# Kernel tuning notes

Hardware: AMD Instinct MI355X
Metric: run time of the kernel (lower is better)

Reference implementation:

```python
import jax, jax.numpy as jnp
import numpy as np

N = 64000      # total nodes in batched graph (16 graphs x 4000)
E = 1024000    # total edges (avg degree 16)
D = 512        # input/output feature dim
KTOT = 2048    # total assign dim (128 clusters per graph)
B = 16         # batch size (number of graphs)


def setup_inputs() -> dict:
    key = jax.random.key(0)
    ks = jax.random.split(key, 5)
    feat = jax.random.normal(ks[0], (N, D), jnp.float32)
    W_feat = jax.random.normal(ks[1], (D, D), jnp.float32) / np.float32(np.sqrt(D))
    b_feat = jnp.zeros((D,), jnp.float32)
    W_pool = jax.random.normal(ks[2], (D, KTOT), jnp.float32) / np.float32(np.sqrt(D))
    b_pool = jnp.zeros((KTOT,), jnp.float32)
    src = jax.random.randint(ks[3], (E,), 0, N, dtype=jnp.int32)
    dst = jax.random.randint(ks[4], (E,), 0, N, dtype=jnp.int32)
    return {"feat": feat, "W_feat": W_feat, "b_feat": b_feat,
            "W_pool": W_pool, "b_pool": b_pool,
            "src": src, "dst": dst, "batch_size": B}


def _gin(x, src, dst, W, b):
    """GIN layer with mean aggregator: relu(W @ (x + mean_neighbors(x)) + b)."""
    n = x.shape[0]
    agg = jax.ops.segment_sum(x[src], dst, num_segments=n)              # [N, d_in]
    deg = jax.ops.segment_sum(jnp.ones((src.shape[0],), x.dtype), dst, num_segments=n)
    agg = agg / jnp.maximum(deg, 1.0)[:, None]
    return jax.nn.relu((x + agg) @ W + b)


def reference(feat, W_feat, b_feat, W_pool, b_pool, src, dst, batch_size):
    n = feat.shape[0]
    ktot = W_pool.shape[1]
    n_per = n // batch_size      # equal-sized graphs (batch_num_nodes)
    k_per = ktot // batch_size   # clusters per graph

    h_feat = _gin(feat, src, dst, W_feat, b_feat)    # [N, D]
    assign = _gin(feat, src, dst, W_pool, b_pool)    # [N, KTOT]

    # block_diag mask: node of graph b may only assign to columns of graph b
    gid_node = jnp.arange(n) // n_per                # [N]
    gid_col = jnp.arange(ktot) // k_per              # [KTOT]
    mask = (gid_node[:, None] == gid_col[None, :]).astype(assign.dtype)

    # allennlp masked_softmax(memory_efficient=False):
    # softmax(x * mask) * mask, renormalized with +1e-13
    s = jax.nn.softmax(assign * mask, axis=-1) * mask
    s = s / (s.sum(axis=-1, keepdims=True) + 1e-13)  # [N, KTOT]

    h = s.T @ h_feat                                 # [KTOT, D]
    # sparse adj @ S via edge-list scatter: (A S)[i] = sum_{(i,j) in E} S[j]
    adj_s = jax.ops.segment_sum(s[dst], src, num_segments=n)  # [N, KTOT]
    adj_new = s.T @ adj_s                            # [KTOT, KTOT]
    return adj_new, h
```

## Files before the change

### kernel.cpp

```cpp
#include <hip/hip_runtime.h>
#include <math.h>

constexpr int N  = 64000;
constexpr int E  = 1024000;
constexpr int D  = 512;
constexpr int KT = 2048;
constexpr int B  = 16;
constexpr int NP = 4000;
constexpr int KP = 128;
constexpr int NR = N / 256;
constexpr int EPB = 2048;
constexpr int NPB = E / EPB;
constexpr int RSTRIDE = 4608;
constexpr int BSTRIDE = 4608;

typedef __attribute__((ext_vector_type(4))) float f32x4;
typedef __attribute__((ext_vector_type(2))) float f32x2;
typedef __attribute__((ext_vector_type(8))) short bf16x8;
typedef __attribute__((ext_vector_type(8))) unsigned short u16x8;

__device__ __forceinline__ unsigned short f2bf(float f) {
    unsigned u = __builtin_bit_cast(unsigned, f);
    return (unsigned short)((u + 0x7FFFu + ((u >> 16) & 1u)) >> 16);
}
__device__ __forceinline__ float bf2f(unsigned short h) {
    unsigned u = (unsigned)h << 16;
    return __builtin_bit_cast(float, u);
}

__device__ __forceinline__ unsigned char f2fp8_sw(float f) {
    unsigned u = __builtin_bit_cast(unsigned, f);
    unsigned s = u >> 31;
    float a = fabsf(f);
    if (a > 448.f) a = 448.f;
    unsigned code;
    if (a < 0.015625f) {
        code = (unsigned)rintf(a * 512.0f);
    } else {
        unsigned au = __builtin_bit_cast(unsigned, a);
        unsigned mant = au & 0x7FFFFFu;
        unsigned rnd = 0x7FFFFu + ((mant >> 20) & 1u);
        unsigned r2 = au + rnd;
        int e = (int)(r2 >> 23) - 127;
        unsigned m3 = (r2 >> 20) & 7u;
        if (e > 8) { e = 8; m3 = 7; }
        code = (unsigned)((e + 7) << 3) | m3;
    }
    return (unsigned char)(code | (s << 7));
}
__device__ __forceinline__ float fp82f_sw(unsigned b) {
    unsigned s = b >> 7, e = (b >> 3) & 15u, m = b & 7u;
    float vn = __builtin_bit_cast(float, ((e + 120u) << 23) | (m << 20));
    float vs = (float)(int)m * 0x1p-9f;
    float v = e ? vn : vs;
    return s ? -v : v;
}

__device__ __forceinline__ unsigned pack4_fp8(float f0, float f1, float f2, float f3) {
#if __has_builtin(__builtin_amdgcn_cvt_pk_fp8_f32)
    int w = __builtin_amdgcn_cvt_pk_fp8_f32(f0, f1, 0, false);
    w = __builtin_amdgcn_cvt_pk_fp8_f32(f2, f3, w, true);
    return (unsigned)w;
#else
    return (unsigned)f2fp8_sw(f0) | ((unsigned)f2fp8_sw(f1) << 8) |
           ((unsigned)f2fp8_sw(f2) << 16) | ((unsigned)f2fp8_sw(f3) << 24);
#endif
}

__device__ __forceinline__ void acc8_fp8(float* a, uint2 w) {
#if __has_builtin(__builtin_amdgcn_cvt_pk_f32_fp8)
    f32x2 p0 = __builtin_amdgcn_cvt_pk_f32_fp8((int)w.x, false);
    f32x2 p1 = __builtin_amdgcn_cvt_pk_f32_fp8((int)w.x, true);
    f32x2 p2 = __builtin_amdgcn_cvt_pk_f32_fp8((int)w.y, false);
    f32x2 p3 = __builtin_amdgcn_cvt_pk_f32_fp8((int)w.y, true);
    a[0] += p0.x; a[1] += p0.y; a[2] += p1.x; a[3] += p1.y;
    a[4] += p2.x; a[5] += p2.y; a[6] += p3.x; a[7] += p3.y;
#else
    #pragma unroll
    for (int q = 0; q < 4; ++q) a[q] += fp82f_sw((w.x >> (8 * q)) & 255u);
    #pragma unroll
    for (int q = 0; q < 4; ++q) a[4 + q] += fp82f_sw((w.y >> (8 * q)) & 255u);
#endif
}

typedef const __attribute__((address_space(1))) unsigned int* gas_u32p;
typedef __attribute__((address_space(3))) unsigned int* las_u32p;
__device__ __forceinline__ void glds16(const unsigned short* g, unsigned short* l) {
    __builtin_amdgcn_global_load_lds((gas_u32p)(const void*)g, (las_u32p)(void*)l, 16, 0, 0);
}

__device__ __forceinline__ int block_incl_scan(int v, int* ws) {
    int t = threadIdx.x, lane = t & 63, w = t >> 6;
    int x = v;
    #pragma unroll
    for (int off = 1; off < 64; off <<= 1) {
        int y = __shfl_up(x, off);
        if (lane >= off) x += y;
    }
    if (lane == 63) ws[w] = x;
    __syncthreads();
    if (t < 4) {
        int s = ws[t];
        #pragma unroll
        for (int off = 1; off < 4; off <<= 1) {
            int y = __shfl_up(s, off);
            if (t >= off) s += y;
        }
        ws[t] = s;
    }
    __syncthreads();
    return x + (w > 0 ? ws[w - 1] : 0);
}

__global__ __launch_bounds__(256) void k_cvt(const float* __restrict__ in,
                                             unsigned short* __restrict__ outb,
                                             unsigned char* __restrict__ out8,
                                             long long n) {
    long long i = ((long long)blockIdx.x * 256 + threadIdx.x) * 8;
    if (i >= n) return;
    f32x4 a = *(const f32x4*)&in[i];
    f32x4 b = *(const f32x4*)&in[i + 4];
    u16x8 o;
    o[0] = f2bf(a.x); o[1] = f2bf(a.y); o[2] = f2bf(a.z); o[3] = f2bf(a.w);
    o[4] = f2bf(b.x); o[5] = f2bf(b.y); o[6] = f2bf(b.z); o[7] = f2bf(b.w);
    *(u16x8*)&outb[i] = o;
    uint2 w;
    w.x = pack4_fp8(a.x, a.y, a.z, a.w);
    w.y = pack4_fp8(b.x, b.y, b.z, b.w);
    *(uint2*)&out8[i] = w;
}

__global__ void k_zrow(unsigned short* __restrict__ fb,
                       unsigned short* __restrict__ scb,
                       unsigned short* __restrict__ hfb,
                       unsigned char* __restrict__ f8b) {
    int t = threadIdx.x;
    const u16x8 Z = {0, 0, 0, 0, 0, 0, 0, 0};
    if (t < 64)        *(u16x8*)&fb[(size_t)N * D + t * 8] = Z;
    else if (t < 80)   *(u16x8*)&scb[(size_t)N * KP + (t - 64) * 8] = Z;
    else if (t < 144)  *(u16x8*)&hfb[(size_t)N * D + (t - 80) * 8] = Z;
    else if (t < 176)  *(u16x8*)&f8b[(size_t)N * D + (size_t)(t - 144) * 16] = Z;
}

__global__ __launch_bounds__(256) void k_transpose(const float* __restrict__ in,
                                                   unsigned short* __restrict__ out,
                                                   int R, int C) {
    __shared__ float tile[32][33];
    int bx = blockIdx.x * 32, by = blockIdx.y * 32;
    int tx = threadIdx.x & 31, ty = threadIdx.x >> 5;
    #pragma unroll
    for (int i = 0; i < 32; i += 8)
        if (by + ty + i < R && bx + tx < C)
            tile[ty + i][tx] = in[(size_t)(by + ty + i) * C + bx + tx];
    __syncthreads();
    #pragma unroll
    for (int i = 0; i < 32; i += 8)
        if (bx + ty + i < C && by + tx < R)
            out[(size_t)(bx + ty + i) * R + by + tx] = f2bf(tile[tx][ty + i]);
}

__global__ void k_init(int* __restrict__ rcur, int* __restrict__ bcur) {
    int t = threadIdx.x;
    if (t < NR) rcur[t] = t * RSTRIDE;
    bcur[t] = t * BSTRIDE;
}

__global__ __launch_bounds__(256) void k_split(const int* __restrict__ src,
                                               const int* __restrict__ dst,
                                               int* __restrict__ rcur, int2* __restrict__ out1,
                                               int* __restrict__ bcur, int2* __restrict__ out2) {
    __shared__ int2 stg[EPB];
    __shared__ int h[256], lstart[256], gbase[256];
    __shared__ int ws[4];
    int t = threadIdx.x;
    int e0 = blockIdx.x * EPB;
    int sv[8], dv[8], bin[8], rank[8];
    #pragma unroll
    for (int i = 0; i < 8; ++i) {
        int e = e0 + t + i * 256;
        sv[i] = src[e]; dv[i] = dst[e];
    }
    h[t] = 0;
    __syncthreads();
    #pragma unroll
    for (int i = 0; i < 8; ++i) {
        bin[i] = dv[i] >> 8;
        rank[i] = atomicAdd(&h[bin[i]], 1);
    }
    __syncthreads();
    {
        int v = h[t];
        int incl = block_incl_scan(v, ws);
        lstart[t] = incl - v;
        gbase[t] = v ? atomicAdd(&rcur[t], v) : 0;
    }
    __syncthreads();
    #pragma unroll
    for (int i = 0; i < 8; ++i)
        stg[lstart[bin[i]] + rank[i]] = int2{sv[i], dv[i]};
    __syncthreads();
    for (int i = t; i < EPB; i += 256) {
        int2 e = stg[i];
        int b = e.y >> 8;
        out1[gbase[b] + i - lstart[b]] = e;
    }
    __syncthreads();
    h[t] = 0;
    __syncthreads();
    #pragma unroll
    for (int i = 0; i < 8; ++i) {
        bin[i] = (sv[i] / NP) * B + dv[i] / NP;
        rank[i] = atomicAdd(&h[bin[i]], 1);
    }
    __syncthreads();
    {
        int v = h[t];
        int incl = block_incl_scan(v, ws);
        lstart[t] = incl - v;
        gbase[t] = v ? atomicAdd(&bcur[t], v) : 0;
    }
    __syncthreads();
    #pragma unroll
    for (int i = 0; i < 8; ++i)
        stg[lstart[bin[i]] + rank[i]] = int2{sv[i], dv[i]};
    __syncthreads();
    for (int i = t; i < EPB; i += 256) {
        int2 e = stg[i];
        int b = (e.x / NP) * B + e.y / NP;
        out2[gbase[b] + i - lstart[b]] = e;
    }
}

__global__ __launch_bounds__(256) void k_part2(const int2* __restrict__ pairs,
                                               const int* __restrict__ rcur,
                                               int* __restrict__ rowstart,
                                               int* __restrict__ degv,
                                               int* __restrict__ csr) {
    __shared__ int h[256];
    __shared__ int ws[4];
    int t = threadIdx.x;
    int r = blockIdx.x;
    int p0 = r * RSTRIDE, p1 = rcur[r];
    h[t] = 0;
    __syncthreads();
    for (int p = p0 + t; p < p1; p += 256)
        atomicAdd(&h[pairs[p].y & 255], 1);
    __syncthreads();
    int v = h[t];
    int incl = block_incl_scan(v, ws);
    int start = p0 + incl - v;
    __syncthreads();
    h[t] = start;
    rowstart[r * 256 + t] = start;
    degv[r * 256 + t] = v;
    __syncthreads();
    for (int p = p0 + t; p < p1; p += 256) {
        int2 e = pairs[p];
        int pos = atomicAdd(&h[e.y & 255], 1);
        csr[pos] = e.x;
    }
}

__global__ __launch_bounds__(256) void k_agg(const unsigned short* __restrict__ fb,
                                             const unsigned char* __restrict__ f8,
                                             const int* __restrict__ rowstart,
                                             const int* __restrict__ degv,
                                             const int* __restrict__ csr,
                                             unsigned short* __restrict__ xb) {
    int w = threadIdx.x >> 6, lane = threadIdx.x & 63;
    int node = blockIdx.x * 4 + w;
    int r0 = rowstart[node], dg = degv[node], r1 = r0 + dg;
    u16x8 self = *(const u16x8*)&fb[(size_t)node * D + lane * 8];
    float a[8] = {};
    for (int base = r0; base < r1; base += 64) {
        int ii = base + lane;
        int idx = N;
        if (ii < r1) idx = csr[ii];
        int cnt = r1 - base; if (cnt > 64) cnt = 64;
        int batches = (cnt + 7) & ~7;
        for (int j = 0; j < batches; j += 8) {
            int s0 = __shfl(idx, j + 0), s1 = __shfl(idx, j + 1);
            int s2 = __shfl(idx, j + 2), s3 = __shfl(idx, j + 3);
            int s4 = __shfl(idx, j + 4), s5 = __shfl(idx, j + 5);
            int s6 = __shfl(idx, j + 6), s7 = __shfl(idx, j + 7);
            uint2 g0 = *(const uint2*)&f8[(size_t)s0 * D + lane * 8];
            uint2 g1 = *(const uint2*)&f8[(size_t)s1 * D + lane * 8];
            uint2 g2 = *(const uint2*)&f8[(size_t)s2 * D + lane * 8];
            uint2 g3 = *(const uint2*)&f8[(size_t)s3 * D + lane * 8];
            uint2 g4 = *(const uint2*)&f8[(size_t)s4 * D + lane * 8];
            uint2 g5 = *(const uint2*)&f8[(size_t)s5 * D + lane * 8];
            uint2 g6 = *(const uint2*)&f8[(size_t)s6 * D + lane * 8];
            uint2 g7 = *(const uint2*)&f8[(size_t)s7 * D + lane * 8];
            acc8_fp8(a, g0); acc8_fp8(a, g1); acc8_fp8(a, g2); acc8_fp8(a, g3);
            acc8_fp8(a, g4); acc8_fp8(a, g5); acc8_fp8(a, g6); acc8_fp8(a, g7);
        }
    }
    float inv = 1.0f / fmaxf((float)dg, 1.0f);
    u16x8 o;
    #pragma unroll
    for (int q = 0; q < 8; ++q) o[q] = f2bf(bf2f(self[q]) + a[q] * inv);
    *(u16x8*)&xb[(size_t)node * D + lane * 8] = o;
}

__global__ __launch_bounds__(256) void k_gemm_feat(const unsigned short* __restrict__ Xb,
                                                   const unsigned short* __restrict__ Wt,
                                                   const float* __restrict__ bias,
                                                   unsigned short* __restrict__ Hf) {
    __shared__ unsigned short As[128 * 64];
    __shared__ unsigned short Bs[128 * 64];
    int t = threadIdx.x, wid = t >> 6, lane = t & 63;
    int wm = wid >> 1, wn = wid & 1;
    int row0 = blockIdx.x * 128, col0 = blockIdx.y * 128;
    int r8 = lane >> 3, ch = (lane & 7) ^ r8;
    f32x4 acc[4][4] = {};
    for (int k0 = 0; k0 < D; k0 += 64) {
        #pragma unroll
        for (int i = 0; i < 4; ++i) {
            int rr = wid * 32 + i * 8;
            glds16(Xb + (size_t)(row0 + rr + r8) * D + k0 + ch * 8, As + rr * 64);
            glds16(Wt + (size_t)(col0 + rr + r8) * D + k0 + ch * 8, Bs + rr * 64);
        }
        __syncthreads();
        #pragma unroll
        for (int ks = 0; ks < 2; ++ks) {
            bf16x8 af[4], bfr[4];
            #pragma unroll
            for (int f = 0; f < 4; ++f) {
                int ra = wm * 64 + f * 16 + (lane & 15);
                af[f] = *(const bf16x8*)&As[ra * 64 + (((ks * 4 + (lane >> 4)) ^ (ra & 7)) << 3)];
                int rb = wn * 64 + f * 16 + (lane & 15);
                bfr[f] = *(const bf16x8*)&Bs[rb * 64 + (((ks * 4 + (lane >> 4)) ^ (rb & 7)) << 3)];
            }
            #pragma unroll
            for (int m = 0; m < 4; ++m)
                #pragma unroll
                for (int n = 0; n < 4; ++n)
                    acc[m][n] = __builtin_amdgcn_mfma_f32_16x16x32_bf16(af[m], bfr[n], acc[m][n], 0, 0, 0);
        }
        __syncthreads();
    }
    float bv[4];
    #pragma unroll
    for (int n = 0; n < 4; ++n) bv[n] = bias[col0 + wn * 64 + n * 16 + (lane & 15)];
    #pragma unroll
    for (int m = 0; m < 4; ++m)
        #pragma unroll
        for (int r = 0; r < 4; ++r) {
            int row = row0 + wm * 64 + m * 16 + (lane >> 4) * 4 + r;
            #pragma unroll
            for (int n = 0; n < 4; ++n) {
                int col = col0 + wn * 64 + n * 16 + (lane & 15);
                float v = fmaxf(acc[m][n][r] + bv[n], 0.f);
                Hf[(size_t)row * D + col] = f2bf(v);
            }
        }
}

__global__ __launch_bounds__(256) void k_gemm_pool(const unsigned short* __restrict__ Xb,
                                                   const unsigned short* __restrict__ Wpt,
                                                   const float* __restrict__ bp,
                                                   unsigned short* __restrict__ sc) {
    __shared__ unsigned short As[128 * 64];
    __shared__ unsigned short Bs[128 * 64];
    int t = threadIdx.x, wid = t >> 6, lane = t & 63;
    int bm = blockIdx.x;
    int g  = blockIdx.y;
    int row0 = g * NP + bm * 128;
    int nrows = NP - bm * 128; if (nrows > 128) nrows = 128;
    int col0 = g * KP;
    int r8 = lane >> 3, ch = (lane & 7) ^ r8;
    f32x4 acc[2][8] = {};
    for (int k0 = 0; k0 < D; k0 += 64) {
        #pragma unroll
        for (int i = 0; i < 4; ++i) {
            int rr = wid * 32 + i * 8;
            glds16(Xb + (size_t)(row0 + rr + r8) * D + k0 + ch * 8, As + rr * 64);
            glds16(Wpt + (size_t)(col0 + rr + r8) * D + k0 + ch * 8, Bs + rr * 64);
        }
        __syncthreads();
        #pragma unroll
        for (int ks = 0; ks < 2; ++ks) {
            bf16x8 af[2], bfr[8];
            #pragma unroll
            for (int m = 0; m < 2; ++m) {
                int ra = wid * 32 + m * 16 + (lane & 15);
                af[m] = *(const bf16x8*)&As[ra * 64 + (((ks * 4 + (lane >> 4)) ^ (ra & 7)) << 3)];
            }
            #pragma unroll
            for (int n = 0; n < 8; ++n) {
                int rb = n * 16 + (lane & 15);
                bfr[n] = *(const bf16x8*)&Bs[rb * 64 + (((ks * 4 + (lane >> 4)) ^ (rb & 7)) << 3)];
            }
            #pragma unroll
            for (int m = 0; m < 2; ++m)
                #pragma unroll
                for (int n = 0; n < 8; ++n)
                    acc[m][n] = __builtin_amdgcn_mfma_f32_16x16x32_bf16(af[m], bfr[n], acc[m][n], 0, 0, 0);
        }
        __syncthreads();
    }
    float bv[8];
    #pragma unroll
    for (int n = 0; n < 8; ++n) bv[n] = bp[col0 + n * 16 + (lane & 15)];
    #pragma unroll
    for (int m = 0; m < 2; ++m)
        #pragma unroll
        for (int r = 0; r < 4; ++r) {
            float v[8];
            #pragma unroll
            for (int n = 0; n < 8; ++n) v[n] = fmaxf(acc[m][n][r] + bv[n], 0.f);
            float mx = v[0];
            #pragma unroll
            for (int n = 1; n < 8; ++n) mx = fmaxf(mx, v[n]);
            #pragma unroll
            for (int off = 1; off < 16; off <<= 1) mx = fmaxf(mx, __shfl_xor(mx, off));
            float ssum = 0.f;
            #pragma unroll
            for (int n = 0; n < 8; ++n) { v[n] = __expf(v[n] - mx); ssum += v[n]; }
            #pragma unroll
            for (int off = 1; off < 16; off <<= 1) ssum += __shfl_xor(ssum, off);
            float inv = 1.0f / ssum;
            int rowl = wid * 32 + m * 16 + (lane >> 4) * 4 + r;
            if (rowl < nrows) {
                #pragma unroll
                for (int n = 0; n < 8; ++n)
                    sc[(size_t)(row0 + rowl) * KP + n * 16 + (lane & 15)] = f2bf(v[n] * inv);
            }
        }
}

constexpr int VBASE = 4128;

__device__ __forceinline__ void uv_write(unsigned short* arr, int c0, int es,
                                         const u16x8& l0, const u16x8& l1,
                                         const u16x8& l2, const u16x8& l3) {
    #pragma unroll
    for (int q = 0; q < 8; ++q) {
        int r0 = c0 + q, r1 = c0 + 8 + q, r2 = c0 + 16 + q, r3 = c0 + 24 + q;
        arr[r0 * 32 + (es ^ (((r0 >> 1) & 3) << 3))] = l0[q];
        arr[r1 * 32 + (es ^ (((r1 >> 1) & 3) << 3))] = l1[q];
        arr[r2 * 32 + (es ^ (((r2 >> 1) & 3) << 3))] = l2[q];
        arr[r3 * 32 + (es ^ (((r3 >> 1) & 3) << 3))] = l3[q];
    }
}

__device__ __forceinline__ void row_load(const unsigned short* row,
                                         u16x8& l0, u16x8& l1, u16x8& l2, u16x8& l3) {
    l0 = *(const u16x8*)(row);
    l1 = *(const u16x8*)(row + 8);
    l2 = *(const u16x8*)(row + 16);
    l3 = *(const u16x8*)(row + 24);
}

__device__ __forceinline__ bf16x8 uv_read(const unsigned short* UV, int base,
                                          int row, int chunk) {
    int c = chunk ^ ((row >> 1) & 3);
    return *(const bf16x8*)&UV[base + row * 32 + c * 8];
}

constexpr int KZ_H = 16;
__global__ __launch_bounds__(256) void k_h(const unsigned short* __restrict__ sc,
                                           const unsigned short* __restrict__ hf,
                                           float* __restrict__ outH) {
    __shared__ __align__(16) unsigned short UV[8224];
    int t = threadIdx.x, wid = t >> 6, lane = t & 63;
    int g  = blockIdx.x;
    int nt = blockIdx.y;
    int kz = blockIdx.z;
    int n0 = nt * 128;
    int i0 = g * NP + kz * (NP / KZ_H), i1 = i0 + NP / KZ_H;
    int c0 = wid * 32;
    int es = lane & 31, op = lane >> 5;
    unsigned short* arr = &UV[op * VBASE];
    f32x4 acc[2][8] = {};

    const unsigned short* baseptr = op ? (hf + n0 + c0) : (sc + c0);
    int rstride = op ? D : KP;
    auto mkrow = [&](int tbase) -> const unsigned short* {
        int nd = tbase + es;
        nd = nd < i1 ? nd : N;
        return baseptr + (size_t)nd * rstride;
    };

    u16x8 a0, a1, a2, a3, b0, b1, b2, b3;
    row_load(mkrow(i0), a0, a1, a2, a3);
    row_load(mkrow(i0 + 32), b0, b1, b2, b3);

    int ntile = (i1 - i0 + 31) >> 5;
    for (int tt = 0; tt < ntile; tt += 2) {
        __syncthreads();
        uv_write(arr, c0, es, a0, a1, a2, a3);
        __syncthreads();
        row_load(mkrow(i0 + (tt + 2) * 32), a0, a1, a2, a3);
        {
            bf16x8 af[2], bfr[8];
            #pragma unroll
            for (int m = 0; m < 2; ++m)
                af[m] = uv_read(UV, 0, wid * 32 + m * 16 + (lane & 15), lane >> 4);
            #pragma unroll
            for (int n = 0; n < 8; ++n)
                bfr[n] = uv_read(UV, VBASE, n * 16 + (lane & 15), lane >> 4);
            #pragma unroll
            for (int m = 0; m < 2; ++m)
                #pragma unroll
                for (int n = 0; n < 8; ++n)
                    acc[m][n] = __builtin_amdgcn_mfma_f32_16x16x32_bf16(af[m], bfr[n], acc[m][n], 0, 0, 0);
        }
        __syncthreads();
        uv_write(arr, c0, es, b0, b1, b2, b3);
        __syncthreads();
        row_load(mkrow(i0 + (tt + 3) * 32), b0, b1, b2, b3);
        {
            bf16x8 af[2], bfr[8];
            #pragma unroll
            for (int m = 0; m < 2; ++m)
                af[m] = uv_read(UV, 0, wid * 32 + m * 16 + (lane & 15), lane >> 4);
            #pragma unroll
            for (int n = 0; n < 8; ++n)
                bfr[n] = uv_read(UV, VBASE, n * 16 + (lane & 15), lane >> 4);
            #pragma unroll
            for (int m = 0; m < 2; ++m)
                #pragma unroll
                for (int n = 0; n < 8; ++n)
                    acc[m][n] = __builtin_amdgcn_mfma_f32_16x16x32_bf16(af[m], bfr[n], acc[m][n], 0, 0, 0);
        }
    }
    #pragma unroll
    for (int m = 0; m < 2; ++m)
        #pragma unroll
        for (int r = 0; r < 4; ++r) {
            int row = g * KP + wid * 32 + m * 16 + (lane >> 4) * 4 + r;
            #pragma unroll
            for (int n = 0; n < 8; ++n) {
                int col = n0 + n * 16 + (lane & 15);
                atomicAdd(&outH[(size_t)row * D + col], acc[m][n][r]);
            }
        }
}

constexpr int ADJ_SPLIT = 4;
__global__ __launch_bounds__(256) void k_adj(const unsigned short* __restrict__ sc,
                                             const int2* __restrict__ bpairs,
                                             const int* __restrict__ bcur,
                                             float* __restrict__ outA) {
    __shared__ __align__(16) unsigned short UV[8224];
    int t = threadIdx.x, wid = t >> 6, lane = t & 63;
    int b = blockIdx.x, part = blockIdx.y;
    int g1 = b >> 4, g2 = b & 15;
    int e0 = b * BSTRIDE, e1 = bcur[b], cnt = e1 - e0;
    int s0 = e0 + (int)((long long)cnt * part / ADJ_SPLIT);
    int s1 = e0 + (int)((long long)cnt * (part + 1) / ADJ_SPLIT);
    int c0 = wid * 32;
    int es = lane & 31, op = lane >> 5;
    unsigned short* arr = &UV[op * VBASE];
    f32x4 acc[2][8] = {};

    auto mkrow = [&](int tbase) -> const unsigned short* {
        int idx = tbase + es;
        bool v = idx < s1;
        int2 e = bpairs[v ? idx : s0];
        int node = v ? (op ? e.y : e.x) : N;
        return sc + (size_t)node * KP + c0;
    };

    u16x8 a0, a1, a2, a3, b0, b1, b2, b3;
    row_load(mkrow(s0), a0, a1, a2, a3);
    row_load(mkrow(s0 + 32), b0, b1, b2, b3);

    int ntile = (s1 - s0 + 31) >> 5;
    for (int tt = 0; tt < ntile; tt += 2) {
        __syncthreads();
        uv_write(arr, c0, es, a0, a1, a2, a3);
        __syncthreads();
        row_load(mkrow(s0 + (tt + 2) * 32), a0, a1, a2, a3);
        {
            bf16x8 af[2], bfr[8];
            #pragma unroll
            for (int m = 0; m < 2; ++m)
                af[m] = uv_read(UV, 0, wid * 32 + m * 16 + (lane & 15), lane >> 4);
            #pragma unroll
            for (int n = 0; n < 8; ++n)
                bfr[n] = uv_read(UV, VBASE, n * 16 + (lane & 15), lane >> 4);
            #pragma unroll
            for (int m = 0; m < 2; ++m)
                #pragma unroll
                for (int n = 0; n < 8; ++n)
                    acc[m][n] = __builtin_amdgcn_mfma_f32_16x16x32_bf16(af[m], bfr[n], acc[m][n], 0, 0, 0);
        }
        __syncthreads();
        uv_write(arr, c0, es, b0, b1, b2, b3);
        __syncthreads();
        row_load(mkrow(s0 + (tt + 3) * 32), b0, b1, b2, b3);
        {
            bf16x8 af[2], bfr[8];
            #pragma unroll
            for (int m = 0; m < 2; ++m)
                af[m] = uv_read(UV, 0, wid * 32 + m * 16 + (lane & 15), lane >> 4);
            #pragma unroll
            for (int n = 0; n < 8; ++n)
                bfr[n] = uv_read(UV, VBASE, n * 16 + (lane & 15), lane >> 4);
            #pragma unroll
            for (int m = 0; m < 2; ++m)
                #pragma unroll
                for (int n = 0; n < 8; ++n)
                    acc[m][n] = __builtin_amdgcn_mfma_f32_16x16x32_bf16(af[m], bfr[n], acc[m][n], 0, 0, 0);
        }
    }
    #pragma unroll
    for (int m = 0; m < 2; ++m)
        #pragma unroll
        for (int r = 0; r < 4; ++r) {
            int row = g1 * KP + wid * 32 + m * 16 + (lane >> 4) * 4 + r;
            #pragma unroll
            for (int n = 0; n < 8; ++n) {
                int col = g2 * KP + n * 16 + (lane & 15);
                atomicAdd(&outA[(size_t)row * KT + col], acc[m][n][r]);
            }
        }
}

extern "C" void kernel_launch(void* const* d_in, const int* in_sizes, int n_in,
                              void* d_out, int out_size, void* d_ws, size_t ws_size,
                              hipStream_t stream) {
    const float* feat   = (const float*)d_in[0];
    const float* W_feat = (const float*)d_in[1];
    const float* b_feat = (const float*)d_in[2];
    const float* W_pool = (const float*)d_in[3];
    const float* b_pool = (const float*)d_in[4];
    const int*   src    = (const int*)d_in[5];
    const int*   dst    = (const int*)d_in[6];

    char* w = (char*)d_ws;
    unsigned short* fb  = (unsigned short*)w; w += (size_t)(N + 1) * D * 2;
    unsigned char*  f8b = (unsigned char*)w;  w += (size_t)(N + 1) * D;
    unsigned short* xb  = (unsigned short*)w; w += (size_t)N * D * 2;
    unsigned short* hfb = (unsigned short*)w; w += (size_t)(N + 1) * D * 2;
    unsigned short* scb = (unsigned short*)w; w += (size_t)(N + 1) * KP * 2;
    unsigned short* Wt  = (unsigned short*)w; w += (size_t)D * D * 2;
    unsigned short* Wpt = (unsigned short*)w; w += (size_t)KT * D * 2;
    int2* pairs1  = (int2*)w; w += (size_t)NR * RSTRIDE * 8;
    int2* bpairs  = (int2*)w; w += (size_t)256 * BSTRIDE * 8;
    int*  csr     = (int*)w;  w += ((size_t)NR * RSTRIDE + 64) * 4;
    int*  rowstart= (int*)w;  w += (size_t)N * 4;
    int*  degv    = (int*)w;  w += (size_t)N * 4;
    int*  rcur    = (int*)w;  w += NR * 4;
    int*  bcur    = (int*)w;  w += 256 * 4;

    hipMemsetAsync(d_out, 0, (size_t)out_size * sizeof(float), stream);

    k_cvt<<<(int)(((long long)N * D) / (8 * 256)), 256, 0, stream>>>(feat, fb, f8b, (long long)N * D);
    k_zrow<<<1, 256, 0, stream>>>(fb, scb, hfb, f8b);
    dim3 gt1(D / 32, D / 32);
    k_transpose<<<gt1, 256, 0, stream>>>(W_feat, Wt, D, D);
    dim3 gt2(KT / 32, D / 32);
    k_transpose<<<gt2, 256, 0, stream>>>(W_pool, Wpt, D, KT);

    k_init<<<1, 256, 0, stream>>>(rcur, bcur);
    k_split<<<NPB, 256, 0, stream>>>(src, dst, rcur, pairs1, bcur, bpairs);
    k_part2<<<NR, 256, 0, stream>>>(pairs1, rcur, rowstart, degv, csr);

    k_agg<<<N / 4, 256, 0, stream>>>(fb, f8b, rowstart, degv, csr, xb);
    dim3 gf(N / 128, D / 128);
    k_gemm_feat<<<gf, 256, 0, stream>>>(xb, Wt, b_feat, hfb);
    dim3 gp(32, B);
    k_gemm_pool<<<gp, 256, 0, stream>>>(xb, Wpt, b_pool, scb);
    dim3 gh(B, D / 128, KZ_H);
    k_h<<<gh, 256, 0, stream>>>(scb, hfb, (float*)d_out + (size_t)KT * KT);
    dim3 ga(256, ADJ_SPLIT);
    k_adj<<<ga, 256, 0, stream>>>(scb, bpairs, bcur, (float*)d_out);
}
```

Before: 449.7 us.

## Fuse h and adjacency pooling kernels into one interleaved launch

```diff
diff --git a/kernel.cpp b/kernel.cpp
--- a/kernel.cpp
+++ b/kernel.cpp
@@ -430,6 +430,8 @@
 }
 
 constexpr int VBASE = 4128;
+constexpr int ADJ_SPLIT = 4;
+constexpr int KZ_H = 16;
 
 __device__ __forceinline__ void uv_write(unsigned short* arr, int c0, int es,
                                          const u16x8& l0, const u16x8& l1,
@@ -458,15 +460,12 @@
     return *(const bf16x8*)&UV[base + row * 32 + c * 8];
 }
 
-constexpr int KZ_H = 16;
-__global__ __launch_bounds__(256) void k_h(const unsigned short* __restrict__ sc,
-                                           const unsigned short* __restrict__ hf,
-                                           float* __restrict__ outH) {
-    __shared__ __align__(16) unsigned short UV[8224];
+__device__ __forceinline__ void h_body(unsigned short* UV,
+                                       const unsigned short* __restrict__ sc,
+                                       const unsigned short* __restrict__ hf,
+                                       float* __restrict__ outH,
+                                       int g, int nt, int kz) {
     int t = threadIdx.x, wid = t >> 6, lane = t & 63;
-    int g  = blockIdx.x;
-    int nt = blockIdx.y;
-    int kz = blockIdx.z;
     int n0 = nt * 128;
     int i0 = g * NP + kz * (NP / KZ_H), i1 = i0 + NP / KZ_H;
     int c0 = wid * 32;
@@ -538,15 +537,14 @@
         }
 }
 
-constexpr int ADJ_SPLIT = 4;
-__global__ __launch_bounds__(256) void k_adj(const unsigned short* __restrict__ sc,
-                                             const int2* __restrict__ bpairs,
-                                             const int* __restrict__ bcur,
-                                             float* __restrict__ outA) {
-    __shared__ __align__(16) unsigned short UV[8224];
+__device__ __forceinline__ void adj_body(unsigned short* UV,
+                                         const unsigned short* __restrict__ sc,
+                                         const int2* __restrict__ bpairs,
+                                         const int* __restrict__ bcur,
+                                         float* __restrict__ outA,
+                                         int g1, int g2, int part) {
     int t = threadIdx.x, wid = t >> 6, lane = t & 63;
-    int b = blockIdx.x, part = blockIdx.y;
-    int g1 = b >> 4, g2 = b & 15;
+    int b = g1 * B + g2;
     int e0 = b * BSTRIDE, e1 = bcur[b], cnt = e1 - e0;
     int s0 = e0 + (int)((long long)cnt * part / ADJ_SPLIT);
     int s1 = e0 + (int)((long long)cnt * (part + 1) / ADJ_SPLIT);
@@ -617,6 +615,27 @@
                 atomicAdd(&outA[(size_t)row * KT + col], acc[m][n][r]);
             }
         }
+}
+
+__global__ __launch_bounds__(256, 4) void k_ha(const unsigned short* __restrict__ sc,
+                                               const unsigned short* __restrict__ hf,
+                                               const int2* __restrict__ bpairs,
+                                               const int* __restrict__ bcur,
+                                               float* __restrict__ outH,
+                                               float* __restrict__ outA) {
+    __shared__ __align__(16) unsigned short UV[8224];
+    int lin = blockIdx.x;
+    int k = lin >> 8, rem = lin & 255;
+    if ((k & 1) == 0) {
+        int g1 = (rem & 7) + (((rem >> 7) & 1) << 3);
+        int g2 = (rem >> 3) & 15;
+        int part = k >> 1;
+        adj_body(UV, sc, bpairs, bcur, outA, g1, g2, part);
+    } else {
+        int hidx = (k >> 1) * 256 + rem;
+        int g = hidx & 15, nt = (hidx >> 4) & 3, kz = hidx >> 6;
+        h_body(UV, sc, hf, outH, g, nt, kz);
+    }
 }
 
 extern "C" void kernel_launch(void* const* d_in, const int* in_sizes, int n_in,
@@ -664,8 +683,7 @@
     k_gemm_feat<<<gf, 256, 0, stream>>>(xb, Wt, b_feat, hfb);
     dim3 gp(32, B);
     k_gemm_pool<<<gp, 256, 0, stream>>>(xb, Wpt, b_pool, scb);
-    dim3 gh(B, D / 128, KZ_H);
-    k_h<<<gh, 256, 0, stream>>>(scb, hfb, (float*)d_out + (size_t)KT * KT);
-    dim3 ga(256, ADJ_SPLIT);
-    k_adj<<<ga, 256, 0, stream>>>(scb, bpairs, bcur, (float*)d_out);
-}
+
+    k_ha<<<2048, 256, 0, stream>>>(scb, hfb, bpairs, bcur,
+                                   (float*)d_out + (size_t)KT * KT, (float*)d_out);
+}
```

Result: slower. 488.3 us (+8.6%).
